# Kernel tuning notes

Hardware: AMD Instinct MI355X
Metric: run time of the kernel (lower is better)

## Reference

```python
import jax, jax.numpy as jnp
import numpy as np

EPS = 1e-5
SLOPE = 0.2


def setup_inputs() -> dict:
    key = jax.random.key(0)
    ks = jax.random.split(key, 8)
    B, D, N = 8, 60, 1024
    dims = [(64, 120), (64, 64), (128, 64), (256, 128), (256, 512), (1024, 256)]
    inp = {"x": jax.random.normal(ks[0], (B, D, N), dtype=jnp.float32)}
    for i, (o, c) in enumerate(dims, 1):
        inp[f"w{i}"] = jax.random.normal(ks[i], (o, c), dtype=jnp.float32) / np.sqrt(c).astype(np.float32)
        inp[f"b{i}"] = jnp.zeros((o,), jnp.float32)
        inp[f"g{i}"] = jnp.ones((o,), jnp.float32)
        inp[f"be{i}"] = jnp.zeros((o,), jnp.float32)
    inp["k"] = 20
    return inp


def knn_idx(x, k):
    # x: [B, D, N] -> idx [B, N, k] of nearest neighbors (negative sq dist topk)
    inner = -2.0 * jnp.einsum('bdn,bdm->bnm', x, x)
    xx = jnp.sum(x * x, axis=1)  # [B, N]
    pd = -xx[:, :, None] - inner - xx[:, None, :]
    _, idx = jax.lax.top_k(pd, k)
    return idx


def get_graph_feature(x, k):
    # x: [B, D, N] -> [B, 2D, N, k]
    B, D, N = x.shape
    idx = knn_idx(x, k)  # [B, N, k]
    xt = jnp.transpose(x, (0, 2, 1))  # [B, N, D]
    nbr = xt[jnp.arange(B)[:, None, None], idx]  # [B, N, k, D]
    ctr = xt[:, :, None, :]  # [B, N, 1, D]
    feat = jnp.concatenate([nbr - ctr, jnp.broadcast_to(ctr, nbr.shape)], axis=-1)
    return jnp.transpose(feat, (0, 3, 1, 2))  # [B, 2D, N, k]


def lrelu(x):
    return jnp.where(x >= 0, x, SLOPE * x)


def bn(x, g, b, axes):
    # training-mode batch norm (biased variance), channel axis = 1
    m = jnp.mean(x, axis=axes, keepdims=True)
    v = jnp.mean((x - m) ** 2, axis=axes, keepdims=True)
    sh = [1] * x.ndim
    sh[1] = -1
    return (x - m) * jax.lax.rsqrt(v + EPS) * g.reshape(sh) + b.reshape(sh)


def conv2d1x1(x, w, b):
    return jnp.einsum('bcnk,oc->bonk', x, w) + b[None, :, None, None]


def conv1d1x1(x, w, b):
    return jnp.einsum('bcn,oc->bon', x, w) + b[None, :, None]


def reference(x, w1, b1, g1, be1, w2, b2, g2, be2, w3, b3, g3, be3,
              w4, b4, g4, be4, w5, b5, g5, be5, w6, b6, g6, be6, k):
    h = get_graph_feature(x, k)                             # [B,120,N,k]
    h = lrelu(bn(conv2d1x1(h, w1, b1), g1, be1, (0, 2, 3)))
    x1 = jnp.max(h, axis=-1)
    h = lrelu(bn(conv2d1x1(h, w2, b2), g2, be2, (0, 2, 3)))
    x2 = jnp.max(h, axis=-1)
    h = lrelu(bn(conv2d1x1(h, w3, b3), g3, be3, (0, 2, 3)))
    x3 = jnp.max(h, axis=-1)
    h = lrelu(bn(conv2d1x1(h, w4, b4), g4, be4, (0, 2, 3)))
    x4 = jnp.max(h, axis=-1)
    h = jnp.concatenate([x1, x2, x3, x4], axis=1)           # [B,512,N]
    h = lrelu(bn(conv1d1x1(h, w5, b5), g5, be5, (0, 2)))
    h = lrelu(bn(conv1d1x1(h, w6, b6), g6, be6, (0, 2)))
    return jnp.transpose(h, (0, 2, 1))                      # [B,N,emb_dims]
```

## Files before the change

### kernel.cpp

```cpp
#include <hip/hip_runtime.h>
#include <hip/hip_bf16.h>
#include <math.h>

#define B_ 8
#define D_ 60
#define N_ 1024
#define K_ 20
#define P1_ 8192
#define P2_ 163840

typedef __attribute__((ext_vector_type(8))) short bf16x8;
typedef __attribute__((ext_vector_type(4))) short bf16x4;
typedef __attribute__((ext_vector_type(4))) float f32x4;

__device__ inline float b2f(short s) { return __uint_as_float(((unsigned)(unsigned short)s) << 16); }
__device__ inline short f2b(float f) { __hip_bfloat16 h = __float2bfloat16(f); return *(short*)&h; }
__device__ inline unsigned fenc(float f) { unsigned b = __float_as_uint(f); return (b & 0x80000000u) ? ~b : (b | 0x80000000u); }
__device__ inline float fdec(unsigned k) { return __uint_as_float((k & 0x80000000u) ? (k ^ 0x80000000u) : ~k); }

#define OFF_IDX   0ull
#define OFF_XX    655360ull
#define OFF_STATS 688128ull
#define OFF_XT    720896ull
#define OFF_WB    1769472ull
#define OFF_XC    2662400ull
#define OFF_H5    11051008ull
#define OFF_H6    15245312ull
#define OFF_UV    32022528ull
#define OFF_XR1   36216832ull
#define OFF_XR2   38313984ull
#define OFF_XR3   40411136ull
#define OFF_XR4   44605440ull
#define OFF_H1    52994048ull
#define OFF_H2    73965568ull
#define OFF_H3    94937088ull
#define OFF_PART  136880128ull
#define OFF_PART2 139501568ull

#define WO1 0
#define WO2 8192
#define WO3 12288
#define WO4 20480
#define WO5 53248
#define WO6 184320

#define SO1 0
#define SO2 64
#define SO3 128
#define SO4 256
#define SO5 512
#define SO6 768
#define NCH_TOT 1792

__global__ __launch_bounds__(256) void k_xx(const float* __restrict__ x,
                                            float* __restrict__ xx) {
  int bn = blockIdx.x * 256 + threadIdx.x;
  int b = bn >> 10, n = bn & 1023;
  const float* xb = x + (size_t)b * D_ * N_ + n;
  float s = 0.f;
  for (int d = 0; d < D_; ++d) { float v = xb[(size_t)d * N_]; s += v * v; }
  xx[bn] = s;
}

__global__ __launch_bounds__(256) void k_pd(const float* __restrict__ x,
                                            const float* __restrict__ xx,
                                            float* __restrict__ pd) {
  __shared__ float lnn[D_][64];
  __shared__ float lmm[D_][128];
  int tid = threadIdx.x;
  int m0 = blockIdx.x * 128, n0 = blockIdx.y * 64, b = blockIdx.z;
  const float* xb = x + (size_t)b * D_ * N_;
  #pragma unroll
  for (int i = 0; i < 15; ++i) {
    int idx = tid + i * 256;
    int d = idx >> 6, col = idx & 63;
    lnn[d][col] = xb[(size_t)d * N_ + n0 + col];
  }
  #pragma unroll
  for (int i = 0; i < 30; ++i) {
    int idx = tid + i * 256;
    int d = idx >> 7, col = idx & 127;
    lmm[d][col] = xb[(size_t)d * N_ + m0 + col];
  }
  __syncthreads();
  int tn = tid >> 5, tm = tid & 31;
  float acc[8][4];
  #pragma unroll
  for (int i = 0; i < 8; ++i)
    #pragma unroll
    for (int j = 0; j < 4; ++j) acc[i][j] = 0.f;
  for (int d = 0; d < D_; ++d) {
    f32x4 mv  = *(const f32x4*)&lmm[d][tm * 4];
    f32x4 nva = *(const f32x4*)&lnn[d][tn * 8];
    f32x4 nvb = *(const f32x4*)&lnn[d][tn * 8 + 4];
    #pragma unroll
    for (int i = 0; i < 4; ++i)
      #pragma unroll
      for (int j = 0; j < 4; ++j) {
        acc[i][j]     = fmaf(nva[i], mv[j], acc[i][j]);
        acc[4 + i][j] = fmaf(nvb[i], mv[j], acc[4 + i][j]);
      }
  }
  const float* xxb = xx + b * 1024;
  f32x4 xxm = *(const f32x4*)(xxb + m0 + tm * 4);
  #pragma unroll
  for (int i = 0; i < 8; ++i) {
    int n = n0 + tn * 8 + i;
    float xxn = xxb[n];
    f32x4 o;
    #pragma unroll
    for (int j = 0; j < 4; ++j) o[j] = 2.f * acc[i][j] - xxn - xxm[j];
    *(f32x4*)(pd + ((size_t)(b * 1024 + n) * 1024) + m0 + tm * 4) = o;
  }
}

__global__ __launch_bounds__(256) void k_sel(const float* __restrict__ pd,
                                             int* __restrict__ idxb) {
  int tid = threadIdx.x;
  int wave = tid >> 6, lane = tid & 63;
  int bn = blockIdx.x * 4 + wave;
  const float* row = pd + (size_t)bn * 1024;
  int mbase = lane * 16;
  f32x4 r0 = *(const f32x4*)(row + mbase);
  f32x4 r1 = *(const f32x4*)(row + mbase + 4);
  f32x4 r2 = *(const f32x4*)(row + mbase + 8);
  f32x4 r3 = *(const f32x4*)(row + mbase + 12);
  float v[16];
  #pragma unroll
  for (int j = 0; j < 4; ++j) { v[j] = r0[j]; v[4 + j] = r1[j]; v[8 + j] = r2[j]; v[12 + j] = r3[j]; }
  int* outp = idxb + (size_t)bn * K_;
  for (int kk = 0; kk < K_; ++kk) {
    float bv = v[0]; int bj = 0;
    #pragma unroll
    for (int j = 1; j < 16; ++j)
      if (v[j] > bv) { bv = v[j]; bj = j; }
    int bi = mbase + bj;
    #pragma unroll
    for (int off = 1; off < 64; off <<= 1) {
      float ov = __shfl_xor(bv, off);
      int   oi = __shfl_xor(bi, off);
      if (ov > bv || (ov == bv && oi < bi)) { bv = ov; bi = oi; }
    }
    if (lane == 0) outp[kk] = bi;
    #pragma unroll
    for (int j = 0; j < 16; ++j)
      if (bi == mbase + j) v[j] = -INFINITY;
  }
}

__global__ __launch_bounds__(256) void k_xt(const float* __restrict__ x,
                                            short* __restrict__ xt) {
  int bn = blockIdx.x * 256 + threadIdx.x;
  int b = bn >> 10, n = bn & 1023;
  const float* xb = x + (size_t)b * D_ * N_ + n;
  short* row = xt + (size_t)bn * 64;
  for (int c = 0; c < 60; ++c) row[c] = f2b(xb[(size_t)c * N_]);
  row[60] = 0; row[61] = 0; row[62] = 0; row[63] = 0;
}

__global__ __launch_bounds__(256) void k_wuv(const float* __restrict__ w1,
                                             const float* __restrict__ b1,
                                             short* __restrict__ wuv,
                                             float* __restrict__ buv) {
  int t = blockIdx.x * 256 + threadIdx.x;
  int o = t >> 6, c = t & 63;
  float v = 0.f;
  if (o < 64) { if (c < 60) v = w1[o * 120 + c]; }
  else { int o2 = o - 64; if (c < 60) v = w1[o2 * 120 + 60 + c] - w1[o2 * 120 + c]; }
  wuv[t] = f2b(v);
  if (t < 128) buv[t] = (t < 64) ? 0.f : b1[t - 64];
}

__global__ __launch_bounds__(256) void k_wcvt(const float* __restrict__ w2,
                                              const float* __restrict__ w3,
                                              const float* __restrict__ w4,
                                              const float* __restrict__ w5,
                                              const float* __restrict__ w6,
                                              short* __restrict__ wbase) {
  int t = blockIdx.x * 256 + threadIdx.x;
  if (t < 4096) wbase[WO2 + t] = f2b(w2[t]);
  else if (t < 12288) wbase[WO3 + (t - 4096)] = f2b(w3[t - 4096]);
  else if (t < 45056) wbase[WO4 + (t - 12288)] = f2b(w4[t - 12288]);
  else if (t < 176128) wbase[WO5 + (t - 45056)] = f2b(w5[t - 45056]);
  else if (t < 438272) wbase[WO6 + (t - 176128)] = f2b(w6[t - 176128]);
}

template <int K, int COUT, bool APPLY, bool STATS, bool WMAX, bool HSTORE, bool F32OUT>
__global__ __launch_bounds__(256) void k_gemm(const short* __restrict__ in,
                                              const short* __restrict__ wb,
                                              const float* __restrict__ bias,
                                              const float* __restrict__ Ain,
                                              const float* __restrict__ Bin,
                                              float* __restrict__ part,
                                              short* __restrict__ out,
                                              unsigned* __restrict__ umax) {
  constexpr int PANEL = (K < 128) ? K : 128;
  constexpr int NPAN = K / PANEL;
  constexpr int CPR = PANEL / 8;
  constexpr int CSH = (CPR == 16) ? 4 : 3;
  constexpr int PK = PANEL + 8;
  constexpr int KS = PANEL / 32;
  constexpr int NX = COUT / 64;
  constexpr int SA = 128 * PK * 2;
  constexpr int SMX = WMAX ? (128 * 68 * 4) : 0;
  constexpr int S1 = (SA > SMX) ? SA : SMX;
  __shared__ __align__(16) char smem[S1 + 64 * PK * 2 + 512];
  short* ldsA = (short*)smem;
  short* ldsW = (short*)(smem + S1);
  float* ls = (float*)(smem + S1 + 64 * PK * 2);
  int tid = threadIdx.x;
  int w = tid >> 6, lane = tid & 63;
  int ln = lane & 15, quad = lane >> 4;
  int bid = blockIdx.y * NX + blockIdx.x;
  int tot = NX * gridDim.y;
  int gid = (bid & 7) * (tot >> 3) + (bid >> 3);
  int bxx = gid % NX;
  int rp = gid / NX;
  int co0 = bxx * 64;
  const short* srcA = in + (size_t)rp * 128 * K;
  const short* srcW = wb + (size_t)co0 * K;

  f32x4 acc[4][2];
  #pragma unroll
  for (int m = 0; m < 4; ++m)
    #pragma unroll
    for (int t = 0; t < 2; ++t) acc[m][t] = (f32x4){0.f, 0.f, 0.f, 0.f};

  for (int pan = 0; pan < NPAN; ++pan) {
    int kp = pan * PANEL;
    if (pan) __syncthreads();
    #pragma unroll
    for (int i = 0; i < CPR / 2; ++i) {
      int g = i * 256 + tid;
      int row = g >> CSH, c = g & (CPR - 1);
      bf16x8 v = *(const bf16x8*)(srcA + (size_t)row * K + kp + c * 8);
      if (APPLY) {
        f32x4 a0 = *(const f32x4*)(Ain + kp + c * 8);
        f32x4 a1 = *(const f32x4*)(Ain + kp + c * 8 + 4);
        f32x4 b0 = *(const f32x4*)(Bin + kp + c * 8);
        f32x4 b1 = *(const f32x4*)(Bin + kp + c * 8 + 4);
        #pragma unroll
        for (int j = 0; j < 8; ++j) {
          float aj = j < 4 ? a0[j] : a1[j - 4];
          float bj = j < 4 ? b0[j] : b1[j - 4];
          float f = b2f(v[j]) * aj + bj;
          f = f >= 0.f ? f : 0.2f * f;
          v[j] = f2b(f);
        }
      }
      *(bf16x8*)(ldsA + row * PK + c * 8) = v;
    }
    #pragma unroll
    for (int i = 0; i < CPR / 4; ++i) {
      int g = i * 256 + tid;
      int row = g >> CSH, c = g & (CPR - 1);
      *(bf16x8*)(ldsW + row * PK + c * 8) =
          *(const bf16x8*)(srcW + (size_t)row * K + kp + c * 8);
    }
    __syncthreads();
    #pragma unroll
    for (int ks = 0; ks < KS; ++ks) {
      bf16x8 a[4], bfr[2];
      #pragma unroll
      for (int m = 0; m < 4; ++m)
        a[m] = *(const bf16x8*)(ldsW + (m * 16 + ln) * PK + ks * 32 + quad * 8);
      #pragma unroll
      for (int t = 0; t < 2; ++t)
        bfr[t] = *(const bf16x8*)(ldsA + (w * 32 + t * 16 + ln) * PK + ks * 32 + quad * 8);
      #pragma unroll
      for (int m = 0; m < 4; ++m)
        #pragma unroll
        for (int t = 0; t < 2; ++t)
          acc[m][t] = __builtin_amdgcn_mfma_f32_16x16x32_bf16(a[m], bfr[t], acc[m][t], 0, 0, 0);
    }
  }
  #pragma unroll
  for (int m = 0; m < 4; ++m) {
    f32x4 bs = *(const f32x4*)(bias + co0 + m * 16 + quad * 4);
    #pragma unroll
    for (int t = 0; t < 2; ++t)
      #pragma unroll
      for (int r = 0; r < 4; ++r) acc[m][t][r] += bs[r];
  }
  if (HSTORE) {
    #pragma unroll
    for (int m = 0; m < 4; ++m)
      #pragma unroll
      for (int t = 0; t < 2; ++t) {
        int p = rp * 128 + w * 32 + t * 16 + ln;
        if (F32OUT) {
          *(f32x4*)((float*)out + (size_t)p * COUT + co0 + m * 16 + quad * 4) = acc[m][t];
        } else {
          bf16x4 o;
          #pragma unroll
          for (int r = 0; r < 4; ++r) o[r] = f2b(acc[m][t][r]);
          *(bf16x4*)(out + (size_t)p * COUT + co0 + m * 16 + quad * 4) = o;
        }
      }
  }
  if (STATS) {
    __syncthreads();
    if (tid < 128) ls[tid] = 0.f;
    __syncthreads();
    #pragma unroll
    for (int m = 0; m < 4; ++m)
      #pragma unroll
      for (int r = 0; r < 4; ++r) {
        float v0 = acc[m][0][r], v1 = acc[m][1][r];
        float s = v0 + v1, ss = v0 * v0 + v1 * v1;
        #pragma unroll
        for (int off = 1; off < 16; off <<= 1) {
          s += __shfl_xor(s, off); ss += __shfl_xor(ss, off);
        }
        if (ln == 0) {
          atomicAdd(&ls[m * 16 + quad * 4 + r], s);
          atomicAdd(&ls[64 + m * 16 + quad * 4 + r], ss);
        }
      }
    __syncthreads();
    if (tid < 128)
      part[((size_t)bxx * gridDim.y + rp) * 128 + tid] = ls[tid];
  }
  if (WMAX) {
    __syncthreads();
    float* m32 = (float*)smem;
    #pragma unroll
    for (int m = 0; m < 4; ++m)
      #pragma unroll
      for (int t = 0; t < 2; ++t)
        *(f32x4*)(m32 + (size_t)(w * 32 + t * 16 + ln) * 68 + m * 16 + quad * 4) = acc[m][t];
    __syncthreads();
    int r0 = rp * 128;
    int pt0 = r0 / 20;
    for (int pr = tid; pr < 512; pr += 256) {
      int lpt = pr >> 6, col = pr & 63;
      int ptg = pt0 + lpt;
      int rs = ptg * 20 - r0, re = rs + 20;
      rs = rs < 0 ? 0 : rs;
      re = re > 128 ? 128 : re;
      if (rs < re) {
        float mv = -INFINITY;
        for (int r = rs; r < re; ++r) mv = fmaxf(mv, m32[r * 68 + col]);
        atomicMax(&umax[(size_t)ptg * COUT + co0 + col], fenc(mv));
      }
    }
  }
}

__global__ __launch_bounds__(256) void k_expand(const float* __restrict__ UVf,
                                                const int* __restrict__ idxb,
                                                short* __restrict__ h1,
                                                float* __restrict__ xr1,
                                                float* __restrict__ part) {
  int tid = threadIdx.x;
  int lp = tid >> 4;
  int c0 = (tid & 15) * 4;
  int pt = blockIdx.x * 16 + lp;
  int base = (pt >> 10) << 10;
  f32x4 V = *(const f32x4*)(UVf + (size_t)pt * 128 + 64 + c0);
  f32x4 sum = (f32x4){0.f, 0.f, 0.f, 0.f};
  f32x4 ssq = (f32x4){0.f, 0.f, 0.f, 0.f};
  f32x4 mx = (f32x4){-INFINITY, -INFINITY, -INFINITY, -INFINITY};
  const int* ip = idxb + (size_t)pt * K_;
  size_t hb = (size_t)pt * K_ * 64 + c0;
  for (int k = 0; k < K_; ++k) {
    int nb = base + ip[k];
    f32x4 U = *(const f32x4*)(UVf + (size_t)nb * 128 + c0);
    bf16x4 o;
    #pragma unroll
    for (int j = 0; j < 4; ++j) {
      float h = U[j] + V[j];
      mx[j] = fmaxf(mx[j], U[j]);
      sum[j] += h; ssq[j] += h * h;
      o[j] = f2b(h);
    }
    *(bf16x4*)(h1 + hb + (size_t)k * 64) = o;
  }
  f32x4 xo;
  #pragma unroll
  for (int j = 0; j < 4; ++j) xo[j] = mx[j] + V[j];
  *(f32x4*)(xr1 + (size_t)pt * 64 + c0) = xo;
  __shared__ float ls[2048];
  *(f32x4*)(ls + tid * 4) = sum;
  *(f32x4*)(ls + 1024 + tid * 4) = ssq;
  __syncthreads();
  if (tid < 32) {
    int cl = tid & 15;
    bool issq = tid >= 16;
    const float* src = ls + (issq ? 1024 : 0);
    f32x4 s = (f32x4){0.f, 0.f, 0.f, 0.f};
    #pragma unroll
    for (int g = 0; g < 16; ++g) {
      f32x4 v = *(const f32x4*)(src + (g * 16 + cl) * 4);
      s[0] += v[0]; s[1] += v[1]; s[2] += v[2]; s[3] += v[3];
    }
    *(f32x4*)(part + (size_t)blockIdx.x * 128 + (issq ? 64 : 0) + cl * 4) = s;
  }
}

__global__ __launch_bounds__(256) void k_red(const float* __restrict__ part, int NB,
                                             float* __restrict__ part2) {
  int cc = blockIdx.x, by = blockIdx.y;
  int tid = threadIdx.x;
  int rg = tid >> 5;
  int c4 = (tid & 31) * 4;
  int chunk = NB >> 5;
  const float* p = part + ((size_t)cc * NB + (size_t)by * chunk) * 128;
  f32x4 acc = (f32x4){0.f, 0.f, 0.f, 0.f};
  for (int r = rg; r < chunk; r += 8) {
    f32x4 v = *(const f32x4*)(p + (size_t)r * 128 + c4);
    acc[0] += v[0]; acc[1] += v[1]; acc[2] += v[2]; acc[3] += v[3];
  }
  __shared__ float lds[1024];
  *(f32x4*)(lds + tid * 4) = acc;
  __syncthreads();
  if (tid < 32) {
    f32x4 s = (f32x4){0.f, 0.f, 0.f, 0.f};
    #pragma unroll
    for (int g = 0; g < 8; ++g) {
      f32x4 v = *(const f32x4*)(lds + (g * 32 + tid) * 4);
      s[0] += v[0]; s[1] += v[1]; s[2] += v[2]; s[3] += v[3];
    }
    *(f32x4*)(part2 + ((size_t)cc * 32 + by) * 128 + tid * 4) = s;
  }
}

__global__ __launch_bounds__(256) void k_bnab(const float* __restrict__ part, int NB,
                                              const float* __restrict__ g,
                                              const float* __restrict__ be,
                                              float* __restrict__ A,
                                              float* __restrict__ Bp, float inv) {
  __shared__ float red[256];
  int tid = threadIdx.x;
  int j = tid & 127, h = tid >> 7;
  const float* p = part + (size_t)blockIdx.x * NB * 128;
  float s = 0.f;
  for (int bx = h; bx < NB; bx += 2) s += p[(size_t)bx * 128 + j];
  red[tid] = s;
  __syncthreads();
  if (tid < 128) red[tid] = red[tid] + red[tid + 128];
  __syncthreads();
  if (tid < 64) {
    int c = blockIdx.x * 64 + tid;
    float m = red[tid] * inv;
    float v = red[64 + tid] * inv - m * m;
    float a = g[c] * rsqrtf(v + 1e-5f);
    A[c] = a; Bp[c] = be[c] - m * a;
  }
}

__global__ __launch_bounds__(256) void k_xcat(const float* __restrict__ xr1,
                                              const unsigned* __restrict__ xr2,
                                              const unsigned* __restrict__ xr3,
                                              const unsigned* __restrict__ xr4,
                                              const float* __restrict__ A,
                                              const float* __restrict__ Bp,
                                              short* __restrict__ xcat) {
  int t = blockIdx.x * 256 + threadIdx.x;
  int p = t >> 7, cq = t & 127;
  int c0 = cq * 4;
  f32x4 v;
  if (c0 < 64) {
    v = *(const f32x4*)(xr1 + (size_t)p * 64 + c0);
  } else {
    const unsigned* src; int cc;
    if (c0 < 128)      { src = xr2 + (size_t)p * 64;  cc = c0 - 64; }
    else if (c0 < 256) { src = xr3 + (size_t)p * 128; cc = c0 - 128; }
    else               { src = xr4 + (size_t)p * 256; cc = c0 - 256; }
    #pragma unroll
    for (int j = 0; j < 4; ++j) v[j] = fdec(src[cc + j]);
  }
  f32x4 a = *(const f32x4*)(A + c0);
  f32x4 b = *(const f32x4*)(Bp + c0);
  bf16x4 o;
  #pragma unroll
  for (int j = 0; j < 4; ++j) {
    float f = v[j] * a[j] + b[j];
    f = f >= 0.f ? f : 0.2f * f;
    o[j] = f2b(f);
  }
  *(bf16x4*)(xcat + (size_t)p * 512 + c0) = o;
}

__global__ __launch_bounds__(256) void k_apply_out(const short* __restrict__ h,
                                                   const float* __restrict__ A,
                                                   const float* __restrict__ Bp,
                                                   float* __restrict__ out) {
  int t = blockIdx.x * 256 + threadIdx.x;
  int c0 = (t & 255) * 4;
  f32x4 a = *(const f32x4*)(A + c0);
  f32x4 b = *(const f32x4*)(Bp + c0);
  bf16x4 v = *(const bf16x4*)(h + (size_t)t * 4);
  f32x4 o;
  #pragma unroll
  for (int r = 0; r < 4; ++r) {
    float f = b2f(v[r]) * a[r] + b[r];
    o[r] = f >= 0.f ? f : 0.2f * f;
  }
  *(f32x4*)(out + (size_t)t * 4) = o;
}

extern "C" void kernel_launch(void* const* d_in, const int* in_sizes, int n_in,
                              void* d_out, int out_size, void* d_ws, size_t ws_size,
                              hipStream_t stream) {
  const float* x   = (const float*)d_in[0];
  const float* w1  = (const float*)d_in[1];
  const float* b1  = (const float*)d_in[2];
  const float* g1  = (const float*)d_in[3];
  const float* be1 = (const float*)d_in[4];
  const float* w2  = (const float*)d_in[5];
  const float* b2  = (const float*)d_in[6];
  const float* g2  = (const float*)d_in[7];
  const float* be2 = (const float*)d_in[8];
  const float* w3  = (const float*)d_in[9];
  const float* b3  = (const float*)d_in[10];
  const float* g3  = (const float*)d_in[11];
  const float* be3 = (const float*)d_in[12];
  const float* w4  = (const float*)d_in[13];
  const float* b4  = (const float*)d_in[14];
  const float* g4  = (const float*)d_in[15];
  const float* be4 = (const float*)d_in[16];
  const float* w5  = (const float*)d_in[17];
  const float* b5  = (const float*)d_in[18];
  const float* g5  = (const float*)d_in[19];
  const float* be5 = (const float*)d_in[20];
  const float* w6  = (const float*)d_in[21];
  const float* b6  = (const float*)d_in[22];
  const float* g6  = (const float*)d_in[23];
  const float* be6 = (const float*)d_in[24];
  float* out = (float*)d_out;
  char* ws = (char*)d_ws;

  int*      idxb = (int*)(ws + OFF_IDX);
  float*    xx   = (float*)(ws + OFF_XX);
  float*    Aall = (float*)(ws + OFF_STATS);
  float*    Ball = Aall + NCH_TOT;
  float*    buv  = Ball + NCH_TOT;
  short*    xt   = (short*)(ws + OFF_XT);
  short*    wbb  = (short*)(ws + OFF_WB);
  short*    xcat = (short*)(ws + OFF_XC);
  short*    h5   = (short*)(ws + OFF_H5);
  short*    h6   = (short*)(ws + OFF_H6);
  float*    UVf  = (float*)(ws + OFF_UV);
  float*    xr1  = (float*)(ws + OFF_XR1);
  unsigned* xr2  = (unsigned*)(ws + OFF_XR2);
  unsigned* xr3  = (unsigned*)(ws + OFF_XR3);
  unsigned* xr4  = (unsigned*)(ws + OFF_XR4);
  short*    h1   = (short*)(ws + OFF_H1);
  short*    h2   = (short*)(ws + OFF_H2);
  short*    h3   = (short*)(ws + OFF_H3);
  float*    pd    = (float*)(ws + OFF_H3);
  float*    part  = (float*)(ws + OFF_PART);
  float*    part2 = (float*)(ws + OFF_PART2);

  hipMemsetAsync(ws + OFF_XR2, 0, 2097152ull + 4194304ull + 8388608ull, stream);

  k_xx <<<P1_ / 256, 256, 0, stream>>>(x, xx);
  k_pd <<<dim3(8, 16, 8), 256, 0, stream>>>(x, xx, pd);
  k_sel<<<P1_ / 4, 256, 0, stream>>>(pd, idxb);
  k_xt <<<P1_ / 256, 256, 0, stream>>>(x, xt);
  k_wuv<<<32, 256, 0, stream>>>(w1, b1, wbb + WO1, buv);
  k_wcvt<<<1712, 256, 0, stream>>>(w2, w3, w4, w5, w6, wbb);

  k_gemm<64, 128, false, false, false, true, true><<<dim3(2, 64), 256, 0, stream>>>(
      xt, wbb + WO1, buv, nullptr, nullptr, nullptr, (short*)UVf, nullptr);
  k_expand<<<P1_ / 16, 256, 0, stream>>>(UVf, idxb, h1, xr1, part);
  k_red <<<dim3(1, 32), 256, 0, stream>>>(part, P1_ / 16, part2);
  k_bnab<<<1, 256, 0, stream>>>(part2, 32, g1, be1, Aall + SO1, Ball + SO1, 1.f / P2_);

  k_gemm<64, 64, true, true, true, true, false><<<dim3(1, P2_ / 128), 256, 0, stream>>>(
      h1, wbb + WO2, b2, Aall + SO1, Ball + SO1, part, h2, xr2);
  k_red <<<dim3(1, 32), 256, 0, stream>>>(part, P2_ / 128, part2);
  k_bnab<<<1, 256, 0, stream>>>(part2, 32, g2, be2, Aall + SO2, Ball + SO2, 1.f / P2_);

  k_gemm<64, 128, true, true, true, true, false><<<dim3(2, P2_ / 128), 256, 0, stream>>>(
      h2, wbb + WO3, b3, Aall + SO2, Ball + SO2, part, h3, xr3);
  k_red <<<dim3(2, 32), 256, 0, stream>>>(part, P2_ / 128, part2);
  k_bnab<<<2, 256, 0, stream>>>(part2, 32, g3, be3, Aall + SO3, Ball + SO3, 1.f / P2_);

  k_gemm<128, 256, true, true, true, false, false><<<dim3(4, P2_ / 128), 256, 0, stream>>>(
      h3, wbb + WO4, b4, Aall + SO3, Ball + SO3, part, nullptr, xr4);
  k_red <<<dim3(4, 32), 256, 0, stream>>>(part, P2_ / 128, part2);
  k_bnab<<<4, 256, 0, stream>>>(part2, 32, g4, be4, Aall + SO4, Ball + SO4, 1.f / P2_);

  k_xcat<<<P1_ * 128 / 256, 256, 0, stream>>>(xr1, xr2, xr3, xr4, Aall, Ball, xcat);

  k_gemm<512, 256, false, true, false, true, false><<<dim3(4, P1_ / 128), 256, 0, stream>>>(
      xcat, wbb + WO5, b5, nullptr, nullptr, part, h5, nullptr);
  k_bnab<<<4, 256, 0, stream>>>(part, P1_ / 128, g5, be5, Aall + SO5, Ball + SO5, 1.f / P1_);

  k_gemm<256, 1024, true, true, false, true, false><<<dim3(16, P1_ / 128), 256, 0, stream>>>(
      h5, wbb + WO6, b6, Aall + SO5, Ball + SO5, part, h6, nullptr);
  k_bnab<<<16, 256, 0, stream>>>(part, P1_ / 128, g6, be6, Aall + SO6, Ball + SO6, 1.f / P1_);
  k_apply_out<<<P1_ * 256 / 256, 256, 0, stream>>>(h6, Aall + SO6, Ball + SO6, out);

  (void)in_sizes; (void)n_in; (void)out_size; (void)ws_size;
}
```

Measured before the change: 439.1 us.

## Shrink GEMM LDS footprint and move BN activation into a separate pass

The GEMM panel is fixed at 64 and the max-reduction staging buffer is no longer sized separately, so it now reuses the A tile and processes the 128 rows in two halves. This lowers shared memory per block and should allow more resident blocks. For the conv4 and conv6 GEMMs, the BN-affine plus leaky-ReLU on the input is moved out of the GEMM load path into a standalone in-place k_act kernel. That adds two extra kernel launches and an extra read/write pass over h3 and h5 in exchange for a simpler GEMM inner loop, and it also adds barriers in the max epilogue.

```diff
diff --git a/kernel.cpp b/kernel.cpp
--- a/kernel.cpp
+++ b/kernel.cpp
@@ -185,6 +185,26 @@
   else if (t < 438272) wbase[WO6 + (t - 176128)] = f2b(w6[t - 176128]);
 }
 
+template <int C>
+__global__ __launch_bounds__(256) void k_act(short* __restrict__ h,
+                                             const float* __restrict__ A,
+                                             const float* __restrict__ Bp) {
+  int t = blockIdx.x * 256 + threadIdx.x;
+  int c0 = (t & (C / 8 - 1)) * 8;
+  bf16x8 v = *(bf16x8*)(h + (size_t)t * 8);
+  f32x4 a0 = *(const f32x4*)(A + c0), a1 = *(const f32x4*)(A + c0 + 4);
+  f32x4 b0 = *(const f32x4*)(Bp + c0), b1 = *(const f32x4*)(Bp + c0 + 4);
+  #pragma unroll
+  for (int j = 0; j < 8; ++j) {
+    float aj = j < 4 ? a0[j] : a1[j - 4];
+    float bj = j < 4 ? b0[j] : b1[j - 4];
+    float f = b2f(v[j]) * aj + bj;
+    f = f >= 0.f ? f : 0.2f * f;
+    v[j] = f2b(f);
+  }
+  *(bf16x8*)(h + (size_t)t * 8) = v;
+}
+
 template <int K, int COUT, bool APPLY, bool STATS, bool WMAX, bool HSTORE, bool F32OUT>
 __global__ __launch_bounds__(256) void k_gemm(const short* __restrict__ in,
                                               const short* __restrict__ wb,
@@ -194,20 +214,18 @@
                                               float* __restrict__ part,
                                               short* __restrict__ out,
                                               unsigned* __restrict__ umax) {
-  constexpr int PANEL = (K < 128) ? K : 128;
+  constexpr int PANEL = 64;
   constexpr int NPAN = K / PANEL;
   constexpr int CPR = PANEL / 8;
-  constexpr int CSH = (CPR == 16) ? 4 : 3;
+  constexpr int CSH = 3;
   constexpr int PK = PANEL + 8;
   constexpr int KS = PANEL / 32;
   constexpr int NX = COUT / 64;
   constexpr int SA = 128 * PK * 2;
-  constexpr int SMX = WMAX ? (128 * 68 * 4) : 0;
-  constexpr int S1 = (SA > SMX) ? SA : SMX;
-  __shared__ __align__(16) char smem[S1 + 64 * PK * 2 + 512];
+  __shared__ __align__(16) char smem[SA + 64 * PK * 2 + 512];
   short* ldsA = (short*)smem;
-  short* ldsW = (short*)(smem + S1);
-  float* ls = (float*)(smem + S1 + 64 * PK * 2);
+  short* ldsW = (short*)(smem + SA);
+  float* ls = (float*)(smem + SA + 64 * PK * 2);
   int tid = threadIdx.x;
   int w = tid >> 6, lane = tid & 63;
   int ln = lane & 15, quad = lane >> 4;
@@ -322,22 +340,26 @@
       part[((size_t)bxx * gridDim.y + rp) * 128 + tid] = ls[tid];
   }
   if (WMAX) {
-    __syncthreads();
     float* m32 = (float*)smem;
     #pragma unroll
-    for (int m = 0; m < 4; ++m)
-      #pragma unroll
-      for (int t = 0; t < 2; ++t)
-        *(f32x4*)(m32 + (size_t)(w * 32 + t * 16 + ln) * 68 + m * 16 + quad * 4) = acc[m][t];
-    __syncthreads();
-    int r0 = rp * 128;
-    int pt0 = r0 / 20;
-    for (int pr = tid; pr < 512; pr += 256) {
-      int lpt = pr >> 6, col = pr & 63;
+    for (int half = 0; half < 2; ++half) {
+      __syncthreads();
+      if ((w >> 1) == half) {
+        int lw = w & 1;
+        #pragma unroll
+        for (int m = 0; m < 4; ++m)
+          #pragma unroll
+          for (int t = 0; t < 2; ++t)
+            *(f32x4*)(m32 + (size_t)(lw * 32 + t * 16 + ln) * 68 + m * 16 + quad * 4) = acc[m][t];
+      }
+      __syncthreads();
+      int r0 = rp * 128 + half * 64;
+      int pt0 = r0 / 20;
+      int lpt = tid >> 6, col = tid & 63;
       int ptg = pt0 + lpt;
       int rs = ptg * 20 - r0, re = rs + 20;
       rs = rs < 0 ? 0 : rs;
-      re = re > 128 ? 128 : re;
+      re = re > 64 ? 64 : re;
       if (rs < re) {
         float mv = -INFINITY;
         for (int r = rs; r < re; ++r) mv = fmaxf(mv, m32[r * 68 + col]);
@@ -578,8 +600,10 @@
   k_red <<<dim3(2, 32), 256, 0, stream>>>(part, P2_ / 128, part2);
   k_bnab<<<2, 256, 0, stream>>>(part2, 32, g3, be3, Aall + SO3, Ball + SO3, 1.f / P2_);
 
-  k_gemm<128, 256, true, true, true, false, false><<<dim3(4, P2_ / 128), 256, 0, stream>>>(
-      h3, wbb + WO4, b4, Aall + SO3, Ball + SO3, part, nullptr, xr4);
+  k_act<128><<<P2_ * 128 / 2048, 256, 0, stream>>>(h3, Aall + SO3, Ball + SO3);
+
+  k_gemm<128, 256, false, true, true, false, false><<<dim3(4, P2_ / 128), 256, 0, stream>>>(
+      h3, wbb + WO4, b4, nullptr, nullptr, part, nullptr, xr4);
   k_red <<<dim3(4, 32), 256, 0, stream>>>(part, P2_ / 128, part2);
   k_bnab<<<4, 256, 0, stream>>>(part2, 32, g4, be4, Aall + SO4, Ball + SO4, 1.f / P2_);
 
@@ -589,8 +613,10 @@
       xcat, wbb + WO5, b5, nullptr, nullptr, part, h5, nullptr);
   k_bnab<<<4, 256, 0, stream>>>(part, P1_ / 128, g5, be5, Aall + SO5, Ball + SO5, 1.f / P1_);
 
-  k_gemm<256, 1024, true, true, false, true, false><<<dim3(16, P1_ / 128), 256, 0, stream>>>(
-      h5, wbb + WO6, b6, Aall + SO5, Ball + SO5, part, h6, nullptr);
+  k_act<256><<<P1_ * 256 / 2048, 256, 0, stream>>>(h5, Aall + SO5, Ball + SO5);
+
+  k_gemm<256, 1024, false, true, false, true, false><<<dim3(16, P1_ / 128), 256, 0, stream>>>(
+      h5, wbb + WO6, b6, nullptr, nullptr, part, h6, nullptr);
   k_bnab<<<16, 256, 0, stream>>>(part, P1_ / 128, g6, be6, Aall + SO6, Ball + SO6, 1.f / P1_);
   k_apply_out<<<P1_ * 256 / 256, 256, 0, stream>>>(h6, Aall + SO6, Ball + SO6, out);
 
```

Result: no change. 436.5 us (-0.6%).

## Load GEMM MFMA fragments directly from global memory with register double-buffering

Applied to the files above, without the earlier changes.

The GEMM kernel no longer stages activation and weight panels through LDS. Each lane now loads its MFMA fragments straight from global memory, ping-ponging two register sets so the next k-slice is fetched while the current one is multiplied. The per-panel barriers and LDS footprint go away, which may raise occupancy. The epilogue also merges the stats and window-max phases under one barrier, with a vectorised 4-wide max. The cost is that weight and activation fragments are re-read from global or L2 by every wave instead of being shared through LDS, and the BN-apply work is duplicated across the waves that share weight tiles.

```diff
diff --git a/kernel.cpp b/kernel.cpp
--- a/kernel.cpp
+++ b/kernel.cpp
@@ -194,20 +194,11 @@
                                               float* __restrict__ part,
                                               short* __restrict__ out,
                                               unsigned* __restrict__ umax) {
-  constexpr int PANEL = (K < 128) ? K : 128;
-  constexpr int NPAN = K / PANEL;
-  constexpr int CPR = PANEL / 8;
-  constexpr int CSH = (CPR == 16) ? 4 : 3;
-  constexpr int PK = PANEL + 8;
-  constexpr int KS = PANEL / 32;
+  constexpr int KT = K / 32;
   constexpr int NX = COUT / 64;
-  constexpr int SA = 128 * PK * 2;
-  constexpr int SMX = WMAX ? (128 * 68 * 4) : 0;
-  constexpr int S1 = (SA > SMX) ? SA : SMX;
-  __shared__ __align__(16) char smem[S1 + 64 * PK * 2 + 512];
-  short* ldsA = (short*)smem;
-  short* ldsW = (short*)(smem + S1);
-  float* ls = (float*)(smem + S1 + 64 * PK * 2);
+  constexpr int MSZ = WMAX ? 128 * 68 : 4;
+  __shared__ __align__(16) float m32s[MSZ];
+  __shared__ float ls[128];
   int tid = threadIdx.x;
   int w = tid >> 6, lane = tid & 63;
   int ln = lane & 15, quad = lane >> 4;
@@ -217,8 +208,9 @@
   int bxx = gid % NX;
   int rp = gid / NX;
   int co0 = bxx * 64;
-  const short* srcA = in + (size_t)rp * 128 * K;
-  const short* srcW = wb + (size_t)co0 * K;
+  const short* pA0 = in + ((size_t)(rp * 128 + w * 32 + ln)) * K + quad * 8;
+  const short* pA1 = pA0 + (size_t)16 * K;
+  const short* pW  = wb + ((size_t)(co0 + ln)) * K + quad * 8;
 
   f32x4 acc[4][2];
   #pragma unroll
@@ -226,54 +218,58 @@
     #pragma unroll
     for (int t = 0; t < 2; ++t) acc[m][t] = (f32x4){0.f, 0.f, 0.f, 0.f};
 
-  for (int pan = 0; pan < NPAN; ++pan) {
-    int kp = pan * PANEL;
-    if (pan) __syncthreads();
-    #pragma unroll
-    for (int i = 0; i < CPR / 2; ++i) {
-      int g = i * 256 + tid;
-      int row = g >> CSH, c = g & (CPR - 1);
-      bf16x8 v = *(const bf16x8*)(srcA + (size_t)row * K + kp + c * 8);
-      if (APPLY) {
-        f32x4 a0 = *(const f32x4*)(Ain + kp + c * 8);
-        f32x4 a1 = *(const f32x4*)(Ain + kp + c * 8 + 4);
-        f32x4 b0 = *(const f32x4*)(Bin + kp + c * 8);
-        f32x4 b1 = *(const f32x4*)(Bin + kp + c * 8 + 4);
-        #pragma unroll
-        for (int j = 0; j < 8; ++j) {
-          float aj = j < 4 ? a0[j] : a1[j - 4];
-          float bj = j < 4 ? b0[j] : b1[j - 4];
-          float f = b2f(v[j]) * aj + bj;
-          f = f >= 0.f ? f : 0.2f * f;
-          v[j] = f2b(f);
-        }
-      }
-      *(bf16x8*)(ldsA + row * PK + c * 8) = v;
-    }
-    #pragma unroll
-    for (int i = 0; i < CPR / 4; ++i) {
-      int g = i * 256 + tid;
-      int row = g >> CSH, c = g & (CPR - 1);
-      *(bf16x8*)(ldsW + row * PK + c * 8) =
-          *(const bf16x8*)(srcW + (size_t)row * K + kp + c * 8);
-    }
-    __syncthreads();
-    #pragma unroll
-    for (int ks = 0; ks < KS; ++ks) {
-      bf16x8 a[4], bfr[2];
+  auto applyv = [&](bf16x8 v, int kc) -> bf16x8 {
+    f32x4 a0 = *(const f32x4*)(Ain + kc);
+    f32x4 a1 = *(const f32x4*)(Ain + kc + 4);
+    f32x4 b0 = *(const f32x4*)(Bin + kc);
+    f32x4 b1 = *(const f32x4*)(Bin + kc + 4);
+    #pragma unroll
+    for (int j = 0; j < 8; ++j) {
+      float aj = j < 4 ? a0[j] : a1[j - 4];
+      float bj = j < 4 ? b0[j] : b1[j - 4];
+      float f = b2f(v[j]) * aj + bj;
+      f = f >= 0.f ? f : 0.2f * f;
+      v[j] = f2b(f);
+    }
+    return v;
+  };
+
+  bf16x8 wf0[4], wf1[4], af0[2], af1[2];
+  #pragma unroll
+  for (int m = 0; m < 4; ++m) wf0[m] = *(const bf16x8*)(pW + (size_t)m * 16 * K);
+  af0[0] = *(const bf16x8*)(pA0);
+  af0[1] = *(const bf16x8*)(pA1);
+  if (APPLY) { af0[0] = applyv(af0[0], quad * 8); af0[1] = applyv(af0[1], quad * 8); }
+
+  for (int kt = 0; kt < KT; kt += 2) {
+    {
+      int off = (kt + 1) * 32;
       #pragma unroll
-      for (int m = 0; m < 4; ++m)
-        a[m] = *(const bf16x8*)(ldsW + (m * 16 + ln) * PK + ks * 32 + quad * 8);
+      for (int m = 0; m < 4; ++m) wf1[m] = *(const bf16x8*)(pW + (size_t)m * 16 * K + off);
+      af1[0] = *(const bf16x8*)(pA0 + off);
+      af1[1] = *(const bf16x8*)(pA1 + off);
+      if (APPLY) { af1[0] = applyv(af1[0], off + quad * 8); af1[1] = applyv(af1[1], off + quad * 8); }
+    }
+    #pragma unroll
+    for (int m = 0; m < 4; ++m) {
+      acc[m][0] = __builtin_amdgcn_mfma_f32_16x16x32_bf16(wf0[m], af0[0], acc[m][0], 0, 0, 0);
+      acc[m][1] = __builtin_amdgcn_mfma_f32_16x16x32_bf16(wf0[m], af0[1], acc[m][1], 0, 0, 0);
+    }
+    if (kt + 2 < KT) {
+      int off = (kt + 2) * 32;
       #pragma unroll
-      for (int t = 0; t < 2; ++t)
-        bfr[t] = *(const bf16x8*)(ldsA + (w * 32 + t * 16 + ln) * PK + ks * 32 + quad * 8);
-      #pragma unroll
-      for (int m = 0; m < 4; ++m)
-        #pragma unroll
-        for (int t = 0; t < 2; ++t)
-          acc[m][t] = __builtin_amdgcn_mfma_f32_16x16x32_bf16(a[m], bfr[t], acc[m][t], 0, 0, 0);
-    }
-  }
+      for (int m = 0; m < 4; ++m) wf0[m] = *(const bf16x8*)(pW + (size_t)m * 16 * K + off);
+      af0[0] = *(const bf16x8*)(pA0 + off);
+      af0[1] = *(const bf16x8*)(pA1 + off);
+      if (APPLY) { af0[0] = applyv(af0[0], off + quad * 8); af0[1] = applyv(af0[1], off + quad * 8); }
+    }
+    #pragma unroll
+    for (int m = 0; m < 4; ++m) {
+      acc[m][0] = __builtin_amdgcn_mfma_f32_16x16x32_bf16(wf1[m], af1[0], acc[m][0], 0, 0, 0);
+      acc[m][1] = __builtin_amdgcn_mfma_f32_16x16x32_bf16(wf1[m], af1[1], acc[m][1], 0, 0, 0);
+    }
+  }
+
   #pragma unroll
   for (int m = 0; m < 4; ++m) {
     f32x4 bs = *(const f32x4*)(bias + co0 + m * 16 + quad * 4);
@@ -298,52 +294,59 @@
         }
       }
   }
+  if (STATS || WMAX) {
+    if (STATS && tid < 128) ls[tid] = 0.f;
+    if (WMAX) {
+      #pragma unroll
+      for (int m = 0; m < 4; ++m)
+        #pragma unroll
+        for (int t = 0; t < 2; ++t)
+          *(f32x4*)(m32s + (size_t)(w * 32 + t * 16 + ln) * 68 + m * 16 + quad * 4) = acc[m][t];
+    }
+    __syncthreads();
+    if (STATS) {
+      #pragma unroll
+      for (int m = 0; m < 4; ++m)
+        #pragma unroll
+        for (int r = 0; r < 4; ++r) {
+          float v0 = acc[m][0][r], v1 = acc[m][1][r];
+          float s = v0 + v1, ss = v0 * v0 + v1 * v1;
+          #pragma unroll
+          for (int off = 1; off < 16; off <<= 1) {
+            s += __shfl_xor(s, off); ss += __shfl_xor(ss, off);
+          }
+          if (ln == 0) {
+            atomicAdd(&ls[m * 16 + quad * 4 + r], s);
+            atomicAdd(&ls[64 + m * 16 + quad * 4 + r], ss);
+          }
+        }
+    }
+    if (WMAX) {
+      int r0 = rp * 128;
+      int pt0 = r0 / 20;
+      int npt = (r0 + 127) / 20 - pt0 + 1;
+      if (tid < npt * 16) {
+        int lpt = tid >> 4, cq = (tid & 15) * 4;
+        int ptg = pt0 + lpt;
+        int rs = ptg * 20 - r0, re = rs + 20;
+        rs = rs < 0 ? 0 : rs;
+        re = re > 128 ? 128 : re;
+        f32x4 mv = (f32x4){-INFINITY, -INFINITY, -INFINITY, -INFINITY};
+        for (int r = rs; r < re; ++r) {
+          f32x4 v = *(const f32x4*)(m32s + (size_t)r * 68 + cq);
+          #pragma unroll
+          for (int j = 0; j < 4; ++j) mv[j] = fmaxf(mv[j], v[j]);
+        }
+        #pragma unroll
+        for (int j = 0; j < 4; ++j)
+          atomicMax(&umax[(size_t)ptg * COUT + co0 + cq + j], fenc(mv[j]));
+      }
+    }
+  }
   if (STATS) {
-    __syncthreads();
-    if (tid < 128) ls[tid] = 0.f;
-    __syncthreads();
-    #pragma unroll
-    for (int m = 0; m < 4; ++m)
-      #pragma unroll
-      for (int r = 0; r < 4; ++r) {
-        float v0 = acc[m][0][r], v1 = acc[m][1][r];
-        float s = v0 + v1, ss = v0 * v0 + v1 * v1;
-        #pragma unroll
-        for (int off = 1; off < 16; off <<= 1) {
-          s += __shfl_xor(s, off); ss += __shfl_xor(ss, off);
-        }
-        if (ln == 0) {
-          atomicAdd(&ls[m * 16 + quad * 4 + r], s);
-          atomicAdd(&ls[64 + m * 16 + quad * 4 + r], ss);
-        }
-      }
     __syncthreads();
     if (tid < 128)
       part[((size_t)bxx * gridDim.y + rp) * 128 + tid] = ls[tid];
-  }
-  if (WMAX) {
-    __syncthreads();
-    float* m32 = (float*)smem;
-    #pragma unroll
-    for (int m = 0; m < 4; ++m)
-      #pragma unroll
-      for (int t = 0; t < 2; ++t)
-        *(f32x4*)(m32 + (size_t)(w * 32 + t * 16 + ln) * 68 + m * 16 + quad * 4) = acc[m][t];
-    __syncthreads();
-    int r0 = rp * 128;
-    int pt0 = r0 / 20;
-    for (int pr = tid; pr < 512; pr += 256) {
-      int lpt = pr >> 6, col = pr & 63;
-      int ptg = pt0 + lpt;
-      int rs = ptg * 20 - r0, re = rs + 20;
-      rs = rs < 0 ? 0 : rs;
-      re = re > 128 ? 128 : re;
-      if (rs < re) {
-        float mv = -INFINITY;
-        for (int r = rs; r < re; ++r) mv = fmaxf(mv, m32[r * 68 + col]);
-        atomicMax(&umax[(size_t)ptg * COUT + co0 + col], fenc(mv));
-      }
-    }
   }
 }
 
```

Result: slower. 477.6 us (+8.8%).
